# Kernel tuning notes

Measured on AMD Instinct MI355X. Metric: run time of the kernel, lower is better.

The kernel has to match this reference:

```python
import jax, jax.numpy as jnp
import numpy as np

N, E, IN_FT, OUT_FT = 20000, 4096, 128, 128


def setup_inputs() -> dict:
    key = jax.random.key(0)
    kx, kh, kw = jax.random.split(key, 3)
    X = jax.random.normal(kx, (N, IN_FT), dtype=jnp.float32)
    H = jax.random.randint(kh, (N, E), 0, 2, dtype=jnp.int32)
    weight = jax.random.normal(kw, (IN_FT, OUT_FT), dtype=jnp.float32) * (1.0 / np.sqrt(IN_FT))
    bias = jnp.zeros((OUT_FT,), dtype=jnp.float32)
    return {"X": X, "H": H, "weight": weight, "bias": bias}


def reference(X, H, weight, bias):
    # Dv^{-1/2} H De^{-1} H^T Dv^{-1/2} X W + b, with diag matrices fused as
    # row/column scalings (same math as the torch.diag @ chain, no NxN temporaries).
    Hf = H.astype(jnp.float32)
    v_deg = jnp.sum(Hf, axis=1)            # [N]
    e_deg = jnp.sum(Hf, axis=0)            # [E]
    v_deg = jnp.where(v_deg > 0, v_deg, 1.0)
    e_deg = jnp.where(e_deg > 0, e_deg, 1.0)
    dv_inv_sqrt = 1.0 / jnp.sqrt(v_deg)    # diag(Dv^-1/2)
    de_inv = 1.0 / e_deg                   # diag(De^-1)
    Y = dv_inv_sqrt[:, None] * X
    T = Hf.T @ Y                           # H^T (...)        [E, in]
    T = de_inv[:, None] * T                # De^-1 (...)
    Z = Hf @ T                             # H (...)          [N, in]
    Z = dv_inv_sqrt[:, None] * Z           # Dv^-1/2 (...)
    out = Z @ weight + bias                # [N, out]
    return out
```

## Files before the change

kernel.cpp:

```cpp
#include <hip/hip_runtime.h>

#define NV 20000
#define NE 4096
#define FT 128
#define NW_E 128
#define NW_V 625
#define PT_STRIDE 632
#define NKC 313

typedef __attribute__((ext_vector_type(8))) short short8v;
typedef __attribute__((ext_vector_type(4))) float float4v;

__device__ __forceinline__ unsigned short f2bf(float f) {
    unsigned u = __float_as_uint(f);
    u += 0x7FFFu + ((u >> 16) & 1u);
    return (unsigned short)(u >> 16);
}
__device__ __forceinline__ int lds_off(int r, int chunk) {
    return r * 128 + ((chunk ^ (r & 7)) << 4);
}
__device__ __forceinline__ uint4 lut_entry(int t) {
    uint4 e;
    e.x = ((t & 1) ? 0x3F80u : 0u) | ((t & 2) ? 0x3F800000u : 0u);
    e.y = ((t & 4) ? 0x3F80u : 0u) | ((t & 8) ? 0x3F800000u : 0u);
    e.z = ((t & 16) ? 0x3F80u : 0u) | ((t & 32) ? 0x3F800000u : 0u);
    e.w = ((t & 64) ? 0x3F80u : 0u) | ((t & 128) ? 0x3F800000u : 0u);
    return e;
}

__global__ __launch_bounds__(256) void k_pack(const int* __restrict__ H,
                                              unsigned* __restrict__ packed,
                                              float* __restrict__ dv) {
    __shared__ int cl[4];
    int t = threadIdx.x, wave = t >> 6, lane = t & 63;
    int row = blockIdx.x * 2 + (wave >> 1);
    int half = wave & 1;
    const uint4* base = reinterpret_cast<const uint4*>(H) + (size_t)row * 1024 + half * 512 + lane * 8;
    unsigned m = 0;
#pragma unroll
    for (int i = 0; i < 8; ++i) {
        uint4 v = base[i];
        m |= (v.x ? 1u : 0u) << (i * 4 + 0);
        m |= (v.y ? 1u : 0u) << (i * 4 + 1);
        m |= (v.z ? 1u : 0u) << (i * 4 + 2);
        m |= (v.w ? 1u : 0u) << (i * 4 + 3);
    }
    packed[(size_t)row * NW_E + half * 64 + lane] = m;
    int c = __popc(m);
    for (int o = 32; o > 0; o >>= 1) c += __shfl_down(c, o, 64);
    if (lane == 0) cl[wave] = c;
    __syncthreads();
    if (t < 2) {
        int d = cl[t * 2] + cl[t * 2 + 1];
        dv[blockIdx.x * 2 + t] = d > 0 ? 1.0f / sqrtf((float)d) : 1.0f;
    }
}

__global__ __launch_bounds__(256) void k_btrans(const unsigned* __restrict__ packed,
                                                unsigned* __restrict__ packedT) {
    int lane = threadIdx.x & 63;
    int w = threadIdx.x >> 6;
    int ew = blockIdx.y * 4 + w;
    int n = blockIdx.x * 64 + lane;
    unsigned wv = (n < NV) ? packed[(size_t)n * NW_E + ew] : 0u;
    unsigned my = 0;
#pragma unroll
    for (int j = 0; j < 32; ++j) {
        unsigned long long m = __ballot(((wv >> j) & 1u) != 0);
        unsigned part = (lane < 32) ? (unsigned)m : (unsigned)(m >> 32);
        if ((lane & 31) == j) my = part;
    }
    int nw = blockIdx.x * 2 + (lane >> 5);
    int e = ew * 32 + (lane & 31);
    if (nw <= 625) packedT[(size_t)e * PT_STRIDE + nw] = my;
}

__global__ __launch_bounds__(256) void k_mid(const unsigned* __restrict__ packedT,
                                             const float* __restrict__ X,
                                             const float* __restrict__ dv,
                                             float* __restrict__ de,
                                             unsigned short* __restrict__ At) {
    int b = blockIdx.x, t = threadIdx.x;
    int wave = t >> 6, lane = t & 63;
    if (b < 1024) {
        int e = b * 4 + wave;
        const unsigned* row = packedT + (size_t)e * PT_STRIDE;
        int c = 0;
        for (int i = lane; i < NW_V; i += 64) c += __popc(row[i]);
        for (int o = 32; o > 0; o >>= 1) c += __shfl_down(c, o, 64);
        if (lane == 0) de[e] = c > 0 ? 1.0f / (float)c : 1.0f;
    } else if (b < 2274) {
        int b2 = b - 1024;
        int f = t & 127;
        int nb = (b2 * 2 + (t >> 7)) * 8;
        unsigned short h[8];
#pragma unroll
        for (int i = 0; i < 8; ++i) {
            int n = nb + i;
            h[i] = f2bf(X[(size_t)n * FT + f] * dv[n]);
        }
        uint4 u;
        u.x = (unsigned)h[0] | ((unsigned)h[1] << 16);
        u.y = (unsigned)h[2] | ((unsigned)h[3] << 16);
        u.z = (unsigned)h[4] | ((unsigned)h[5] << 16);
        u.w = (unsigned)h[6] | ((unsigned)h[7] << 16);
        int kc = nb >> 6;
        *reinterpret_cast<uint4*>(At + (size_t)kc * 8192 + f * 64 + (nb & 63)) = u;
    } else {
        int f = t & 127;
        uint4 z = {0, 0, 0, 0};
        *reinterpret_cast<uint4*>(At + (size_t)312 * 8192 + f * 64 + 32 + (t >> 7) * 8) = z;
        *reinterpret_cast<uint4*>(At + (size_t)312 * 8192 + f * 64 + 48 + (t >> 7) * 8) = z;
    }
}

__global__ __launch_bounds__(256, 2) void k_mm1(const unsigned short* __restrict__ At,
                                                const unsigned* __restrict__ packedT,
                                                float* __restrict__ P, int chunkK) {
    __shared__ __align__(16) unsigned char sA[16384];
    __shared__ __align__(16) unsigned char sB[16384];
    __shared__ __align__(16) uint4 slut[256];
    int t = threadIdx.x;
    slut[t] = lut_entry(t);

    int et = blockIdx.x & 31, kp = blockIdx.x >> 5;
    int e0 = et * 128;
    int kbeg = kp * chunkK;
    int kend = kbeg + chunkK; if (kend > NKC * 64) kend = NKC * 64;
    int iters = (kend - kbeg) >> 6; if (iters < 0) iters = 0;

    float4v acc[4][4];
#pragma unroll
    for (int i = 0; i < 4; ++i)
#pragma unroll
        for (int j = 0; j < 4; ++j)
#pragma unroll
            for (int r = 0; r < 4; ++r) acc[i][j][r] = 0.0f;

    int wave = t >> 6, lane = t & 63;
    int wm0 = (wave & 1) * 64, wc0 = (wave >> 1) * 64;
    int r0 = lane & 15, q = lane >> 4;

    const unsigned* brow = packedT + (size_t)(e0 + (t & 127)) * PT_STRIDE + (kbeg >> 5);
    uint4 bw, bw2;
    if (t < 128) bw = *reinterpret_cast<const uint4*>(brow);
    __syncthreads();

    for (int it = 0; it < iters; ++it) {
        int kc = (kbeg >> 6) + it;
        const uint4* slab = reinterpret_cast<const uint4*>(At + (size_t)kc * 8192);
#pragma unroll
        for (int c = 0; c < 4; ++c) {
            int idx = c * 256 + t;
            uint4 v = slab[idx];
            *reinterpret_cast<uint4*>(sA + lds_off(idx >> 3, idx & 7)) = v;
        }
        if (t < 128) {
            unsigned w0, w1;
            if (!(it & 1)) {
                bw2 = *reinterpret_cast<const uint4*>(brow + 2 * it + 4);
                w0 = bw.x; w1 = bw.y;
            } else {
                w0 = bw.z; w1 = bw.w;
            }
            int rB = t;
#pragma unroll
            for (int c = 0; c < 4; ++c)
                *reinterpret_cast<uint4*>(sB + lds_off(rB, c)) = slut[(w0 >> (c * 8)) & 0xFF];
#pragma unroll
            for (int c = 0; c < 4; ++c)
                *reinterpret_cast<uint4*>(sB + lds_off(rB, 4 + c)) = slut[(w1 >> (c * 8)) & 0xFF];
            if (it & 1) bw = bw2;
        }
        __syncthreads();
#pragma unroll
        for (int ks = 0; ks < 2; ++ks) {
            short8v a[4], bb[4];
#pragma unroll
            for (int mi = 0; mi < 4; ++mi)
                a[mi] = *reinterpret_cast<const short8v*>(sA + lds_off(wm0 + mi * 16 + r0, ks * 4 + q));
#pragma unroll
            for (int ci = 0; ci < 4; ++ci)
                bb[ci] = *reinterpret_cast<const short8v*>(sB + lds_off(wc0 + ci * 16 + r0, ks * 4 + q));
#pragma unroll
            for (int mi = 0; mi < 4; ++mi)
#pragma unroll
                for (int ci = 0; ci < 4; ++ci)
                    acc[mi][ci] = __builtin_amdgcn_mfma_f32_16x16x32_bf16(a[mi], bb[ci], acc[mi][ci], 0, 0, 0);
        }
        __syncthreads();
    }
    float* Pp = P + (size_t)kp * (128 * 4096);
#pragma unroll
    for (int mi = 0; mi < 4; ++mi)
#pragma unroll
        for (int ci = 0; ci < 4; ++ci) {
            int f = wm0 + mi * 16 + q * 4;
            int e = e0 + wc0 + ci * 16 + r0;
#pragma unroll
            for (int r = 0; r < 4; ++r)
                Pp[(size_t)(f + r) * 4096 + e] = acc[mi][ci][r];
        }
}

__global__ __launch_bounds__(256) void k_reduce(const float4v* __restrict__ P,
                                                float4v* __restrict__ Tt, int S) {
    int i = blockIdx.x * 256 + threadIdx.x;
    float4v a = P[i];
    for (int p = 1; p < S; ++p) a += P[(size_t)p * 131072 + i];
    Tt[i] = a;
}

__global__ __launch_bounds__(256) void k_ut(const float* __restrict__ Tt,
                                            const float* __restrict__ W,
                                            const float* __restrict__ de,
                                            unsigned short* __restrict__ Ut) {
    int t = threadIdx.x;
    int bx = blockIdx.x;
    int e = bx * 64 + (t & 63);
    int g0 = blockIdx.y * 16 + (t >> 6) * 4;
    float a0 = 0, a1 = 0, a2 = 0, a3 = 0;
    for (int f = 0; f < 128; ++f) {
        float tv = Tt[(size_t)f * 4096 + e];
        float4 wv = *reinterpret_cast<const float4*>(W + f * 128 + g0);
        a0 += tv * wv.x; a1 += tv * wv.y; a2 += tv * wv.z; a3 += tv * wv.w;
    }
    float d = de[e];
    int j = t & 63;
    Ut[(size_t)bx * 8192 + (g0 + 0) * 64 + j] = f2bf(a0 * d);
    Ut[(size_t)bx * 8192 + (g0 + 1) * 64 + j] = f2bf(a1 * d);
    Ut[(size_t)bx * 8192 + (g0 + 2) * 64 + j] = f2bf(a2 * d);
    Ut[(size_t)bx * 8192 + (g0 + 3) * 64 + j] = f2bf(a3 * d);
}

__global__ __launch_bounds__(256, 4) void k_mm2(const unsigned* __restrict__ packed,
                                                const unsigned short* __restrict__ Ut,
                                                const float* __restrict__ dv,
                                                const float* __restrict__ bias,
                                                float* __restrict__ out) {
    __shared__ __align__(16) unsigned char sA[16384];
    __shared__ __align__(16) unsigned char sB[4096];
    __shared__ __align__(16) uint4 slut[256];
    int t = threadIdx.x;
    slut[t] = lut_entry(t);

    int mt = blockIdx.x >> 2, qg = blockIdx.x & 3;
    int n0 = mt * 128, g0 = qg * 32;

    float4v acc[4];
#pragma unroll
    for (int i = 0; i < 4; ++i)
#pragma unroll
        for (int r = 0; r < 4; ++r) acc[i][r] = 0.0f;

    int wave = t >> 6, lane = t & 63;
    int wm0 = (wave & 1) * 64, wc0 = (wave >> 1) * 16;
    int r0 = lane & 15, q = lane >> 4;

    const unsigned* arow = packed + (size_t)(n0 + (t & 127)) * NW_E;
    const unsigned short* bbase = Ut + (size_t)qg * 2048;
    int t2 = t - 128;
    uint4 aw, aw2;
    if (t < 128) aw = *reinterpret_cast<const uint4*>(arow);
    __syncthreads();

    for (int it = 0; it < 64; ++it) {
        if (t < 128) {
            unsigned w0, w1;
            if (!(it & 1)) {
                aw2 = *reinterpret_cast<const uint4*>(arow + 2 * it + 4);
                w0 = aw.x; w1 = aw.y;
            } else {
                w0 = aw.z; w1 = aw.w;
            }
            int rA = t;
#pragma unroll
            for (int c = 0; c < 4; ++c)
                *reinterpret_cast<uint4*>(sA + lds_off(rA, c)) = slut[(w0 >> (c * 8)) & 0xFF];
#pragma unroll
            for (int c = 0; c < 4; ++c)
                *reinterpret_cast<uint4*>(sA + lds_off(rA, 4 + c)) = slut[(w1 >> (c * 8)) & 0xFF];
            if (it & 1) aw = aw2;
        } else {
            const uint4* src = reinterpret_cast<const uint4*>(bbase + (size_t)it * 8192);
#pragma unroll
            for (int c = 0; c < 2; ++c) {
                int idx = t2 * 2 + c;
                uint4 v = src[idx];
                *reinterpret_cast<uint4*>(sB + lds_off(idx >> 3, idx & 7)) = v;
            }
        }
        __syncthreads();
#pragma unroll
        for (int ks = 0; ks < 2; ++ks) {
            short8v a[4], bb;
#pragma unroll
            for (int mi = 0; mi < 4; ++mi)
                a[mi] = *reinterpret_cast<const short8v*>(sA + lds_off(wm0 + mi * 16 + r0, ks * 4 + q));
            bb = *reinterpret_cast<const short8v*>(sB + lds_off(wc0 + r0, ks * 4 + q));
#pragma unroll
            for (int mi = 0; mi < 4; ++mi)
                acc[mi] = __builtin_amdgcn_mfma_f32_16x16x32_bf16(a[mi], bb, acc[mi], 0, 0, 0);
        }
        __syncthreads();
    }
    {
        int g = g0 + wc0 + r0;
        float bg = bias[g];
#pragma unroll
        for (int mi = 0; mi < 4; ++mi) {
#pragma unroll
            for (int r = 0; r < 4; ++r) {
                int n = n0 + wm0 + mi * 16 + q * 4 + r;
                if (n < NV) out[(size_t)n * 128 + g] = dv[n] * acc[mi][r] + bg;
            }
        }
    }
}

extern "C" void kernel_launch(void* const* d_in, const int* in_sizes, int n_in,
                              void* d_out, int out_size, void* d_ws, size_t ws_size,
                              hipStream_t stream) {
    const float* X    = (const float*)d_in[0];
    const int*   H    = (const int*)d_in[1];
    const float* W    = (const float*)d_in[2];
    const float* bias = (const float*)d_in[3];
    float* out = (float*)d_out;

    char* ws = (char*)d_ws;
    size_t off = 0;
    auto alloc = [&](size_t sz) { char* p = ws + off; off += (sz + 255) & ~(size_t)255; return p; };
    unsigned*       packed  = (unsigned*)alloc((size_t)NV * NW_E * 4);
    unsigned*       packedT = (unsigned*)alloc((size_t)NE * PT_STRIDE * 4);
    unsigned short* At      = (unsigned short*)alloc((size_t)NKC * 8192 * 2);
    float*          Tt      = (float*)alloc((size_t)FT * NE * 4);
    unsigned short* Ut      = (unsigned short*)alloc((size_t)FT * NE * 2);
    float*          dv      = (float*)alloc((size_t)NV * 4);
    float*          de      = (float*)alloc((size_t)NE * 4);
    size_t fixed = off;

    long long avail = (long long)ws_size - (long long)fixed;
    int S = (int)(avail / (128LL * 4096 * 4));
    if (S > 16) S = 16;
    if (S < 1) S = 1;
    float* P1 = (float*)(ws + fixed);
    int chunkK = ((NKC * 64 + S * 64 - 1) / (S * 64)) * 64;

    k_pack  <<<NV / 2, 256, 0, stream>>>(H, packed, dv);
    k_btrans<<<dim3(313, 32), 256, 0, stream>>>(packed, packedT);
    k_mid   <<<2275, 256, 0, stream>>>(packedT, X, dv, de, At);
    k_mm1   <<<32 * S, 256, 0, stream>>>(At, packedT, P1, chunkK);
    k_reduce<<<512, 256, 0, stream>>>((const float4v*)P1, (float4v*)Tt, S);
    k_ut    <<<dim3(64, 8), 256, 0, stream>>>(Tt, W, de, Ut);
    k_mm2   <<<628, 256, 0, stream>>>(packed, Ut, dv, bias, out);
}
```

Baseline: 590.7 us.

## Use direct global-to-LDS loads for dense operands and fold edge degrees into transpose

```diff
diff --git a/kernel.cpp b/kernel.cpp
--- a/kernel.cpp
+++ b/kernel.cpp
@@ -26,6 +26,11 @@
     e.z = ((t & 16) ? 0x3F80u : 0u) | ((t & 32) ? 0x3F800000u : 0u);
     e.w = ((t & 64) ? 0x3F80u : 0u) | ((t & 128) ? 0x3F800000u : 0u);
     return e;
+}
+__device__ __forceinline__ void dma16(const void* g, void* l) {
+    __builtin_amdgcn_global_load_lds(
+        (const __attribute__((address_space(1))) unsigned*)g,
+        (__attribute__((address_space(3))) unsigned*)l, 16, 0, 0);
 }
 
 __global__ __launch_bounds__(256) void k_pack(const int* __restrict__ H,
@@ -57,7 +62,8 @@
 }
 
 __global__ __launch_bounds__(256) void k_btrans(const unsigned* __restrict__ packed,
-                                                unsigned* __restrict__ packedT) {
+                                                unsigned* __restrict__ packedT,
+                                                int* __restrict__ edeg) {
     int lane = threadIdx.x & 63;
     int w = threadIdx.x >> 6;
     int ew = blockIdx.y * 4 + w;
@@ -72,27 +78,19 @@
     }
     int nw = blockIdx.x * 2 + (lane >> 5);
     int e = ew * 32 + (lane & 31);
-    if (nw <= 625) packedT[(size_t)e * PT_STRIDE + nw] = my;
-}
-
-__global__ __launch_bounds__(256) void k_mid(const unsigned* __restrict__ packedT,
-                                             const float* __restrict__ X,
+    if (nw <= 625) {
+        packedT[(size_t)e * PT_STRIDE + nw] = my;
+        if (my) atomicAdd(&edeg[e], __popc(my));
+    }
+}
+
+__global__ __launch_bounds__(256) void k_mid(const float* __restrict__ X,
                                              const float* __restrict__ dv,
-                                             float* __restrict__ de,
                                              unsigned short* __restrict__ At) {
     int b = blockIdx.x, t = threadIdx.x;
-    int wave = t >> 6, lane = t & 63;
-    if (b < 1024) {
-        int e = b * 4 + wave;
-        const unsigned* row = packedT + (size_t)e * PT_STRIDE;
-        int c = 0;
-        for (int i = lane; i < NW_V; i += 64) c += __popc(row[i]);
-        for (int o = 32; o > 0; o >>= 1) c += __shfl_down(c, o, 64);
-        if (lane == 0) de[e] = c > 0 ? 1.0f / (float)c : 1.0f;
-    } else if (b < 2274) {
-        int b2 = b - 1024;
+    if (b < 1250) {
         int f = t & 127;
-        int nb = (b2 * 2 + (t >> 7)) * 8;
+        int nb = (b * 2 + (t >> 7)) * 8;
         unsigned short h[8];
 #pragma unroll
         for (int i = 0; i < 8; ++i) {
@@ -104,13 +102,16 @@
         u.y = (unsigned)h[2] | ((unsigned)h[3] << 16);
         u.z = (unsigned)h[4] | ((unsigned)h[5] << 16);
         u.w = (unsigned)h[6] | ((unsigned)h[7] << 16);
-        int kc = nb >> 6;
-        *reinterpret_cast<uint4*>(At + (size_t)kc * 8192 + f * 64 + (nb & 63)) = u;
+        int kc = nb >> 6, ch = (nb & 63) >> 3;
+        *reinterpret_cast<uint4*>((char*)At + (size_t)kc * 16384 + ch * 2048 + f * 16) = u;
     } else {
-        int f = t & 127;
         uint4 z = {0, 0, 0, 0};
-        *reinterpret_cast<uint4*>(At + (size_t)312 * 8192 + f * 64 + 32 + (t >> 7) * 8) = z;
-        *reinterpret_cast<uint4*>(At + (size_t)312 * 8192 + f * 64 + 48 + (t >> 7) * 8) = z;
+#pragma unroll
+        for (int c = 0; c < 2; ++c) {
+            int idx = t * 2 + c;
+            int ch = 4 + (idx >> 7), f = idx & 127;
+            *reinterpret_cast<uint4*>((char*)At + (size_t)312 * 16384 + ch * 2048 + f * 16) = z;
+        }
     }
 }
 
@@ -148,12 +149,12 @@
 
     for (int it = 0; it < iters; ++it) {
         int kc = (kbeg >> 6) + it;
-        const uint4* slab = reinterpret_cast<const uint4*>(At + (size_t)kc * 8192);
-#pragma unroll
-        for (int c = 0; c < 4; ++c) {
-            int idx = c * 256 + t;
-            uint4 v = slab[idx];
-            *reinterpret_cast<uint4*>(sA + lds_off(idx >> 3, idx & 7)) = v;
+        if (wave >= 2) {
+            const char* slabg = (const char*)At + (size_t)kc * 16384 + (wave - 2) * 8192;
+            char* slabl = (char*)sA + (wave - 2) * 8192;
+#pragma unroll
+            for (int i = 0; i < 8; ++i)
+                dma16(slabg + i * 1024 + lane * 16, slabl + i * 1024);
         }
         if (t < 128) {
             unsigned w0, w1;
@@ -178,7 +179,7 @@
             short8v a[4], bb[4];
 #pragma unroll
             for (int mi = 0; mi < 4; ++mi)
-                a[mi] = *reinterpret_cast<const short8v*>(sA + lds_off(wm0 + mi * 16 + r0, ks * 4 + q));
+                a[mi] = *reinterpret_cast<const short8v*>(sA + (ks * 4 + q) * 2048 + (wm0 + mi * 16 + r0) * 16);
 #pragma unroll
             for (int ci = 0; ci < 4; ++ci)
                 bb[ci] = *reinterpret_cast<const short8v*>(sB + lds_off(wc0 + ci * 16 + r0, ks * 4 + q));
@@ -213,11 +214,10 @@
 
 __global__ __launch_bounds__(256) void k_ut(const float* __restrict__ Tt,
                                             const float* __restrict__ W,
-                                            const float* __restrict__ de,
+                                            const int* __restrict__ edeg,
                                             unsigned short* __restrict__ Ut) {
     int t = threadIdx.x;
-    int bx = blockIdx.x;
-    int e = bx * 64 + (t & 63);
+    int e = blockIdx.x * 64 + (t & 63);
     int g0 = blockIdx.y * 16 + (t >> 6) * 4;
     float a0 = 0, a1 = 0, a2 = 0, a3 = 0;
     for (int f = 0; f < 128; ++f) {
@@ -225,12 +225,15 @@
         float4 wv = *reinterpret_cast<const float4*>(W + f * 128 + g0);
         a0 += tv * wv.x; a1 += tv * wv.y; a2 += tv * wv.z; a3 += tv * wv.w;
     }
-    float d = de[e];
-    int j = t & 63;
-    Ut[(size_t)bx * 8192 + (g0 + 0) * 64 + j] = f2bf(a0 * d);
-    Ut[(size_t)bx * 8192 + (g0 + 1) * 64 + j] = f2bf(a1 * d);
-    Ut[(size_t)bx * 8192 + (g0 + 2) * 64 + j] = f2bf(a2 * d);
-    Ut[(size_t)bx * 8192 + (g0 + 3) * 64 + j] = f2bf(a3 * d);
+    int dgi = edeg[e];
+    float d = dgi > 0 ? 1.0f / (float)dgi : 1.0f;
+    int ec = e >> 6, ch = (e & 63) >> 3, e7 = e & 7;
+    int qg = g0 >> 5, gg0 = g0 & 31;
+    size_t base = (size_t)ec * 8192 + qg * 2048 + ch * 256 + e7;
+    Ut[base + (gg0 + 0) * 8] = f2bf(a0 * d);
+    Ut[base + (gg0 + 1) * 8] = f2bf(a1 * d);
+    Ut[base + (gg0 + 2) * 8] = f2bf(a2 * d);
+    Ut[base + (gg0 + 3) * 8] = f2bf(a3 * d);
 }
 
 __global__ __launch_bounds__(256, 4) void k_mm2(const unsigned* __restrict__ packed,
@@ -258,14 +261,14 @@
     int r0 = lane & 15, q = lane >> 4;
 
     const unsigned* arow = packed + (size_t)(n0 + (t & 127)) * NW_E;
-    const unsigned short* bbase = Ut + (size_t)qg * 2048;
-    int t2 = t - 128;
+    const char* bbase = (const char*)Ut + (size_t)qg * 4096 + wave * 1024;
     uint4 aw, aw2;
-    if (t < 128) aw = *reinterpret_cast<const uint4*>(arow);
+    if (t >= 128) aw = *reinterpret_cast<const uint4*>(arow);
     __syncthreads();
 
     for (int it = 0; it < 64; ++it) {
-        if (t < 128) {
+        dma16(bbase + (size_t)it * 16384 + lane * 16, (char*)sB + wave * 1024);
+        if (t >= 128) {
             unsigned w0, w1;
             if (!(it & 1)) {
                 aw2 = *reinterpret_cast<const uint4*>(arow + 2 * it + 4);
@@ -273,7 +276,7 @@
             } else {
                 w0 = aw.z; w1 = aw.w;
             }
-            int rA = t;
+            int rA = t & 127;
 #pragma unroll
             for (int c = 0; c < 4; ++c)
                 *reinterpret_cast<uint4*>(sA + lds_off(rA, c)) = slut[(w0 >> (c * 8)) & 0xFF];
@@ -281,14 +284,6 @@
             for (int c = 0; c < 4; ++c)
                 *reinterpret_cast<uint4*>(sA + lds_off(rA, 4 + c)) = slut[(w1 >> (c * 8)) & 0xFF];
             if (it & 1) aw = aw2;
-        } else {
-            const uint4* src = reinterpret_cast<const uint4*>(bbase + (size_t)it * 8192);
-#pragma unroll
-            for (int c = 0; c < 2; ++c) {
-                int idx = t2 * 2 + c;
-                uint4 v = src[idx];
-                *reinterpret_cast<uint4*>(sB + lds_off(idx >> 3, idx & 7)) = v;
-            }
         }
         __syncthreads();
 #pragma unroll
@@ -297,7 +292,7 @@
 #pragma unroll
             for (int mi = 0; mi < 4; ++mi)
                 a[mi] = *reinterpret_cast<const short8v*>(sA + lds_off(wm0 + mi * 16 + r0, ks * 4 + q));
-            bb = *reinterpret_cast<const short8v*>(sB + lds_off(wc0 + r0, ks * 4 + q));
+            bb = *reinterpret_cast<const short8v*>(sB + (ks * 4 + q) * 512 + (wc0 + r0) * 16);
 #pragma unroll
             for (int mi = 0; mi < 4; ++mi)
                 acc[mi] = __builtin_amdgcn_mfma_f32_16x16x32_bf16(a[mi], bb, acc[mi], 0, 0, 0);
@@ -336,7 +331,7 @@
     float*          Tt      = (float*)alloc((size_t)FT * NE * 4);
     unsigned short* Ut      = (unsigned short*)alloc((size_t)FT * NE * 2);
     float*          dv      = (float*)alloc((size_t)NV * 4);
-    float*          de      = (float*)alloc((size_t)NE * 4);
+    int*            edeg    = (int*)alloc((size_t)NE * 4);
     size_t fixed = off;
 
     long long avail = (long long)ws_size - (long long)fixed;
@@ -346,11 +341,12 @@
     float* P1 = (float*)(ws + fixed);
     int chunkK = ((NKC * 64 + S * 64 - 1) / (S * 64)) * 64;
 
+    hipMemsetAsync(edeg, 0, (size_t)NE * 4, stream);
     k_pack  <<<NV / 2, 256, 0, stream>>>(H, packed, dv);
-    k_btrans<<<dim3(313, 32), 256, 0, stream>>>(packed, packedT);
-    k_mid   <<<2275, 256, 0, stream>>>(packedT, X, dv, de, At);
+    k_btrans<<<dim3(313, 32), 256, 0, stream>>>(packed, packedT, edeg);
+    k_mid   <<<1251, 256, 0, stream>>>(X, dv, At);
     k_mm1   <<<32 * S, 256, 0, stream>>>(At, packedT, P1, chunkK);
     k_reduce<<<512, 256, 0, stream>>>((const float4v*)P1, (float4v*)Tt, S);
-    k_ut    <<<dim3(64, 8), 256, 0, stream>>>(Tt, W, de, Ut);
+    k_ut    <<<dim3(64, 8), 256, 0, stream>>>(Tt, W, edeg, Ut);
     k_mm2   <<<628, 256, 0, stream>>>(packed, Ut, dv, bias, out);
 }
```

New measurement: 654.6 us. +10.8%, slower.

## Expand bit-packed incidence to bf16 in registers and fuse edge-degree count

Applied to the files above, without the earlier changes.

```diff
diff --git a/kernel.cpp b/kernel.cpp
--- a/kernel.cpp
+++ b/kernel.cpp
@@ -19,13 +19,16 @@
 __device__ __forceinline__ int lds_off(int r, int chunk) {
     return r * 128 + ((chunk ^ (r & 7)) << 4);
 }
-__device__ __forceinline__ uint4 lut_entry(int t) {
-    uint4 e;
-    e.x = ((t & 1) ? 0x3F80u : 0u) | ((t & 2) ? 0x3F800000u : 0u);
-    e.y = ((t & 4) ? 0x3F80u : 0u) | ((t & 8) ? 0x3F800000u : 0u);
-    e.z = ((t & 16) ? 0x3F80u : 0u) | ((t & 32) ? 0x3F800000u : 0u);
-    e.w = ((t & 64) ? 0x3F80u : 0u) | ((t & 128) ? 0x3F800000u : 0u);
-    return e;
+__device__ __forceinline__ short8v expand8(unsigned b) {
+    union { unsigned u[4]; short8v s; } r;
+#pragma unroll
+    for (int j = 0; j < 4; ++j) {
+        unsigned lo = 0u - (b & 1u);
+        unsigned hi = 0u - (b & 2u);
+        r.u[j] = (lo & 0x3F80u) | (hi & 0x3F800000u);
+        b >>= 2;
+    }
+    return r.s;
 }
 
 __global__ __launch_bounds__(256) void k_pack(const int* __restrict__ H,
@@ -57,7 +60,8 @@
 }
 
 __global__ __launch_bounds__(256) void k_btrans(const unsigned* __restrict__ packed,
-                                                unsigned* __restrict__ packedT) {
+                                                unsigned* __restrict__ packedT,
+                                                int* __restrict__ edeg) {
     int lane = threadIdx.x & 63;
     int w = threadIdx.x >> 6;
     int ew = blockIdx.y * 4 + w;
@@ -72,27 +76,19 @@
     }
     int nw = blockIdx.x * 2 + (lane >> 5);
     int e = ew * 32 + (lane & 31);
-    if (nw <= 625) packedT[(size_t)e * PT_STRIDE + nw] = my;
-}
-
-__global__ __launch_bounds__(256) void k_mid(const unsigned* __restrict__ packedT,
-                                             const float* __restrict__ X,
+    if (nw <= 625) {
+        packedT[(size_t)e * PT_STRIDE + nw] = my;
+        if (my) atomicAdd(&edeg[e], __popc(my));
+    }
+}
+
+__global__ __launch_bounds__(256) void k_mid(const float* __restrict__ X,
                                              const float* __restrict__ dv,
-                                             float* __restrict__ de,
                                              unsigned short* __restrict__ At) {
     int b = blockIdx.x, t = threadIdx.x;
-    int wave = t >> 6, lane = t & 63;
-    if (b < 1024) {
-        int e = b * 4 + wave;
-        const unsigned* row = packedT + (size_t)e * PT_STRIDE;
-        int c = 0;
-        for (int i = lane; i < NW_V; i += 64) c += __popc(row[i]);
-        for (int o = 32; o > 0; o >>= 1) c += __shfl_down(c, o, 64);
-        if (lane == 0) de[e] = c > 0 ? 1.0f / (float)c : 1.0f;
-    } else if (b < 2274) {
-        int b2 = b - 1024;
+    if (b < 1250) {
         int f = t & 127;
-        int nb = (b2 * 2 + (t >> 7)) * 8;
+        int nb = (b * 2 + (t >> 7)) * 8;
         unsigned short h[8];
 #pragma unroll
         for (int i = 0; i < 8; ++i) {
@@ -118,10 +114,8 @@
                                                 const unsigned* __restrict__ packedT,
                                                 float* __restrict__ P, int chunkK) {
     __shared__ __align__(16) unsigned char sA[16384];
-    __shared__ __align__(16) unsigned char sB[16384];
-    __shared__ __align__(16) uint4 slut[256];
+    __shared__ __align__(8) unsigned char sBbits[1024];
     int t = threadIdx.x;
-    slut[t] = lut_entry(t);
 
     int et = blockIdx.x & 31, kp = blockIdx.x >> 5;
     int e0 = et * 128;
@@ -139,12 +133,11 @@
 
     int wave = t >> 6, lane = t & 63;
     int wm0 = (wave & 1) * 64, wc0 = (wave >> 1) * 64;
-    int r0 = lane & 15, q = lane >> 4;
+    int r0 = lane & 15, q = lane >> 4, qs = q * 8;
 
     const unsigned* brow = packedT + (size_t)(e0 + (t & 127)) * PT_STRIDE + (kbeg >> 5);
     uint4 bw, bw2;
     if (t < 128) bw = *reinterpret_cast<const uint4*>(brow);
-    __syncthreads();
 
     for (int it = 0; it < iters; ++it) {
         int kc = (kbeg >> 6) + it;
@@ -156,37 +149,35 @@
             *reinterpret_cast<uint4*>(sA + lds_off(idx >> 3, idx & 7)) = v;
         }
         if (t < 128) {
-            unsigned w0, w1;
+            uint2 wpair;
             if (!(it & 1)) {
                 bw2 = *reinterpret_cast<const uint4*>(brow + 2 * it + 4);
-                w0 = bw.x; w1 = bw.y;
+                wpair.x = bw.x; wpair.y = bw.y;
             } else {
-                w0 = bw.z; w1 = bw.w;
-            }
-            int rB = t;
-#pragma unroll
-            for (int c = 0; c < 4; ++c)
-                *reinterpret_cast<uint4*>(sB + lds_off(rB, c)) = slut[(w0 >> (c * 8)) & 0xFF];
-#pragma unroll
-            for (int c = 0; c < 4; ++c)
-                *reinterpret_cast<uint4*>(sB + lds_off(rB, 4 + c)) = slut[(w1 >> (c * 8)) & 0xFF];
-            if (it & 1) bw = bw2;
+                wpair.x = bw.z; wpair.y = bw.w;
+                bw = bw2;
+            }
+            *reinterpret_cast<uint2*>(sBbits + t * 8) = wpair;
         }
         __syncthreads();
+        uint2 bv[4];
+#pragma unroll
+        for (int ci = 0; ci < 4; ++ci)
+            bv[ci] = *reinterpret_cast<const uint2*>(sBbits + (wc0 + ci * 16 + r0) * 8);
 #pragma unroll
         for (int ks = 0; ks < 2; ++ks) {
-            short8v a[4], bb[4];
+            short8v a[4];
 #pragma unroll
             for (int mi = 0; mi < 4; ++mi)
                 a[mi] = *reinterpret_cast<const short8v*>(sA + lds_off(wm0 + mi * 16 + r0, ks * 4 + q));
 #pragma unroll
-            for (int ci = 0; ci < 4; ++ci)
-                bb[ci] = *reinterpret_cast<const short8v*>(sB + lds_off(wc0 + ci * 16 + r0, ks * 4 + q));
-#pragma unroll
-            for (int mi = 0; mi < 4; ++mi)
-#pragma unroll
-                for (int ci = 0; ci < 4; ++ci)
-                    acc[mi][ci] = __builtin_amdgcn_mfma_f32_16x16x32_bf16(a[mi], bb[ci], acc[mi][ci], 0, 0, 0);
+            for (int ci = 0; ci < 4; ++ci) {
+                unsigned byte = ((ks ? bv[ci].y : bv[ci].x) >> qs) & 0xFFu;
+                short8v bb = expand8(byte);
+#pragma unroll
+                for (int mi = 0; mi < 4; ++mi)
+                    acc[mi][ci] = __builtin_amdgcn_mfma_f32_16x16x32_bf16(a[mi], bb, acc[mi][ci], 0, 0, 0);
+            }
         }
         __syncthreads();
     }
@@ -213,7 +204,7 @@
 
 __global__ __launch_bounds__(256) void k_ut(const float* __restrict__ Tt,
                                             const float* __restrict__ W,
-                                            const float* __restrict__ de,
+                                            const int* __restrict__ edeg,
                                             unsigned short* __restrict__ Ut) {
     int t = threadIdx.x;
     int bx = blockIdx.x;
@@ -225,7 +216,8 @@
         float4 wv = *reinterpret_cast<const float4*>(W + f * 128 + g0);
         a0 += tv * wv.x; a1 += tv * wv.y; a2 += tv * wv.z; a3 += tv * wv.w;
     }
-    float d = de[e];
+    int dgi = edeg[e];
+    float d = dgi > 0 ? 1.0f / (float)dgi : 1.0f;
     int j = t & 63;
     Ut[(size_t)bx * 8192 + (g0 + 0) * 64 + j] = f2bf(a0 * d);
     Ut[(size_t)bx * 8192 + (g0 + 1) * 64 + j] = f2bf(a1 * d);
@@ -238,11 +230,9 @@
                                                 const float* __restrict__ dv,
                                                 const float* __restrict__ bias,
                                                 float* __restrict__ out) {
-    __shared__ __align__(16) unsigned char sA[16384];
+    __shared__ __align__(8) unsigned char sAbits[1024];
     __shared__ __align__(16) unsigned char sB[4096];
-    __shared__ __align__(16) uint4 slut[256];
     int t = threadIdx.x;
-    slut[t] = lut_entry(t);
 
     int mt = blockIdx.x >> 2, qg = blockIdx.x & 3;
     int n0 = mt * 128, g0 = qg * 32;
@@ -255,32 +245,25 @@
 
     int wave = t >> 6, lane = t & 63;
     int wm0 = (wave & 1) * 64, wc0 = (wave >> 1) * 16;
-    int r0 = lane & 15, q = lane >> 4;
+    int r0 = lane & 15, q = lane >> 4, qs = q * 8;
 
     const unsigned* arow = packed + (size_t)(n0 + (t & 127)) * NW_E;
     const unsigned short* bbase = Ut + (size_t)qg * 2048;
     int t2 = t - 128;
     uint4 aw, aw2;
     if (t < 128) aw = *reinterpret_cast<const uint4*>(arow);
-    __syncthreads();
 
     for (int it = 0; it < 64; ++it) {
         if (t < 128) {
-            unsigned w0, w1;
+            uint2 wpair;
             if (!(it & 1)) {
                 aw2 = *reinterpret_cast<const uint4*>(arow + 2 * it + 4);
-                w0 = aw.x; w1 = aw.y;
+                wpair.x = aw.x; wpair.y = aw.y;
             } else {
-                w0 = aw.z; w1 = aw.w;
-            }
-            int rA = t;
-#pragma unroll
-            for (int c = 0; c < 4; ++c)
-                *reinterpret_cast<uint4*>(sA + lds_off(rA, c)) = slut[(w0 >> (c * 8)) & 0xFF];
-#pragma unroll
-            for (int c = 0; c < 4; ++c)
-                *reinterpret_cast<uint4*>(sA + lds_off(rA, 4 + c)) = slut[(w1 >> (c * 8)) & 0xFF];
-            if (it & 1) aw = aw2;
+                wpair.x = aw.z; wpair.y = aw.w;
+                aw = aw2;
+            }
+            *reinterpret_cast<uint2*>(sAbits + t * 8) = wpair;
         } else {
             const uint4* src = reinterpret_cast<const uint4*>(bbase + (size_t)it * 8192);
 #pragma unroll
@@ -291,16 +274,19 @@
             }
         }
         __syncthreads();
+        uint2 av[4];
+#pragma unroll
+        for (int mi = 0; mi < 4; ++mi)
+            av[mi] = *reinterpret_cast<const uint2*>(sAbits + (wm0 + mi * 16 + r0) * 8);
 #pragma unroll
         for (int ks = 0; ks < 2; ++ks) {
-            short8v a[4], bb;
-#pragma unroll
-            for (int mi = 0; mi < 4; ++mi)
-                a[mi] = *reinterpret_cast<const short8v*>(sA + lds_off(wm0 + mi * 16 + r0, ks * 4 + q));
-            bb = *reinterpret_cast<const short8v*>(sB + lds_off(wc0 + r0, ks * 4 + q));
-#pragma unroll
-            for (int mi = 0; mi < 4; ++mi)
-                acc[mi] = __builtin_amdgcn_mfma_f32_16x16x32_bf16(a[mi], bb, acc[mi], 0, 0, 0);
+            short8v bb = *reinterpret_cast<const short8v*>(sB + lds_off(wc0 + r0, ks * 4 + q));
+#pragma unroll
+            for (int mi = 0; mi < 4; ++mi) {
+                unsigned byte = ((ks ? av[mi].y : av[mi].x) >> qs) & 0xFFu;
+                short8v a = expand8(byte);
+                acc[mi] = __builtin_amdgcn_mfma_f32_16x16x32_bf16(a, bb, acc[mi], 0, 0, 0);
+            }
         }
         __syncthreads();
     }
@@ -336,7 +322,7 @@
     float*          Tt      = (float*)alloc((size_t)FT * NE * 4);
     unsigned short* Ut      = (unsigned short*)alloc((size_t)FT * NE * 2);
     float*          dv      = (float*)alloc((size_t)NV * 4);
-    float*          de      = (float*)alloc((size_t)NE * 4);
+    int*            edeg    = (int*)alloc((size_t)NE * 4);
     size_t fixed = off;
 
     long long avail = (long long)ws_size - (long long)fixed;
@@ -346,11 +332,12 @@
     float* P1 = (float*)(ws + fixed);
     int chunkK = ((NKC * 64 + S * 64 - 1) / (S * 64)) * 64;
 
+    hipMemsetAsync(edeg, 0, (size_t)NE * 4, stream);
     k_pack  <<<NV / 2, 256, 0, stream>>>(H, packed, dv);
-    k_btrans<<<dim3(313, 32), 256, 0, stream>>>(packed, packedT);
-    k_mid   <<<2275, 256, 0, stream>>>(packedT, X, dv, de, At);
+    k_btrans<<<dim3(313, 32), 256, 0, stream>>>(packed, packedT, edeg);
+    k_mid   <<<1251, 256, 0, stream>>>(X, dv, At);
     k_mm1   <<<32 * S, 256, 0, stream>>>(At, packedT, P1, chunkK);
     k_reduce<<<512, 256, 0, stream>>>((const float4v*)P1, (float4v*)Tt, S);
-    k_ut    <<<dim3(64, 8), 256, 0, stream>>>(Tt, W, de, Ut);
+    k_ut    <<<dim3(64, 8), 256, 0, stream>>>(Tt, W, edeg, Ut);
     k_mm2   <<<628, 256, 0, stream>>>(packed, Ut, dv, bias, out);
 }
```

Result: slower. 693.7 us (+17.4%).

## Fuse transpose with edge-degree atomics and fold split-K reduce into Ut kernel

Applied to the files above, without the earlier changes.

```diff
diff --git a/kernel.cpp b/kernel.cpp
--- a/kernel.cpp
+++ b/kernel.cpp
@@ -56,61 +56,57 @@
     }
 }
 
-__global__ __launch_bounds__(256) void k_btrans(const unsigned* __restrict__ packed,
-                                                unsigned* __restrict__ packedT) {
-    int lane = threadIdx.x & 63;
-    int w = threadIdx.x >> 6;
-    int ew = blockIdx.y * 4 + w;
-    int n = blockIdx.x * 64 + lane;
-    unsigned wv = (n < NV) ? packed[(size_t)n * NW_E + ew] : 0u;
-    unsigned my = 0;
-#pragma unroll
-    for (int j = 0; j < 32; ++j) {
-        unsigned long long m = __ballot(((wv >> j) & 1u) != 0);
-        unsigned part = (lane < 32) ? (unsigned)m : (unsigned)(m >> 32);
-        if ((lane & 31) == j) my = part;
-    }
-    int nw = blockIdx.x * 2 + (lane >> 5);
-    int e = ew * 32 + (lane & 31);
-    if (nw <= 625) packedT[(size_t)e * PT_STRIDE + nw] = my;
-}
-
-__global__ __launch_bounds__(256) void k_mid(const unsigned* __restrict__ packedT,
-                                             const float* __restrict__ X,
-                                             const float* __restrict__ dv,
-                                             float* __restrict__ de,
-                                             unsigned short* __restrict__ At) {
-    int b = blockIdx.x, t = threadIdx.x;
-    int wave = t >> 6, lane = t & 63;
-    if (b < 1024) {
-        int e = b * 4 + wave;
-        const unsigned* row = packedT + (size_t)e * PT_STRIDE;
-        int c = 0;
-        for (int i = lane; i < NW_V; i += 64) c += __popc(row[i]);
-        for (int o = 32; o > 0; o >>= 1) c += __shfl_down(c, o, 64);
-        if (lane == 0) de[e] = c > 0 ? 1.0f / (float)c : 1.0f;
-    } else if (b < 2274) {
-        int b2 = b - 1024;
-        int f = t & 127;
-        int nb = (b2 * 2 + (t >> 7)) * 8;
-        unsigned short h[8];
-#pragma unroll
-        for (int i = 0; i < 8; ++i) {
-            int n = nb + i;
-            h[i] = f2bf(X[(size_t)n * FT + f] * dv[n]);
-        }
-        uint4 u;
-        u.x = (unsigned)h[0] | ((unsigned)h[1] << 16);
-        u.y = (unsigned)h[2] | ((unsigned)h[3] << 16);
-        u.z = (unsigned)h[4] | ((unsigned)h[5] << 16);
-        u.w = (unsigned)h[6] | ((unsigned)h[7] << 16);
-        int kc = nb >> 6;
-        *reinterpret_cast<uint4*>(At + (size_t)kc * 8192 + f * 64 + (nb & 63)) = u;
+__global__ __launch_bounds__(256) void k_prep(const unsigned* __restrict__ packed,
+                                              const float* __restrict__ X,
+                                              const float* __restrict__ dv,
+                                              unsigned* __restrict__ packedT,
+                                              int* __restrict__ edeg,
+                                              unsigned short* __restrict__ At) {
+    int v = blockIdx.x, t = threadIdx.x;
+    if (v < 10016) {
+        int bx = v % 313, by = v / 313;
+        int lane = t & 63;
+        int w = t >> 6;
+        int ew = by * 4 + w;
+        int n = bx * 64 + lane;
+        unsigned wv = (n < NV) ? packed[(size_t)n * NW_E + ew] : 0u;
+        unsigned my = 0;
+#pragma unroll
+        for (int j = 0; j < 32; ++j) {
+            unsigned long long m = __ballot(((wv >> j) & 1u) != 0);
+            unsigned part = (lane < 32) ? (unsigned)m : (unsigned)(m >> 32);
+            if ((lane & 31) == j) my = part;
+        }
+        int nw = bx * 2 + (lane >> 5);
+        int e = ew * 32 + (lane & 31);
+        if (nw <= 625) {
+            packedT[(size_t)e * PT_STRIDE + nw] = my;
+            if (my) atomicAdd(&edeg[e], __popc(my));
+        }
     } else {
-        int f = t & 127;
-        uint4 z = {0, 0, 0, 0};
-        *reinterpret_cast<uint4*>(At + (size_t)312 * 8192 + f * 64 + 32 + (t >> 7) * 8) = z;
-        *reinterpret_cast<uint4*>(At + (size_t)312 * 8192 + f * 64 + 48 + (t >> 7) * 8) = z;
+        int b = v - 10016;
+        if (b < 1250) {
+            int f = t & 127;
+            int nb = (b * 2 + (t >> 7)) * 8;
+            unsigned short h[8];
+#pragma unroll
+            for (int i = 0; i < 8; ++i) {
+                int n = nb + i;
+                h[i] = f2bf(X[(size_t)n * FT + f] * dv[n]);
+            }
+            uint4 u;
+            u.x = (unsigned)h[0] | ((unsigned)h[1] << 16);
+            u.y = (unsigned)h[2] | ((unsigned)h[3] << 16);
+            u.z = (unsigned)h[4] | ((unsigned)h[5] << 16);
+            u.w = (unsigned)h[6] | ((unsigned)h[7] << 16);
+            int kc = nb >> 6;
+            *reinterpret_cast<uint4*>(At + (size_t)kc * 8192 + f * 64 + (nb & 63)) = u;
+        } else {
+            int f = t & 127;
+            uint4 z = {0, 0, 0, 0};
+            *reinterpret_cast<uint4*>(At + (size_t)312 * 8192 + f * 64 + 32 + (t >> 7) * 8) = z;
+            *reinterpret_cast<uint4*>(At + (size_t)312 * 8192 + f * 64 + 48 + (t >> 7) * 8) = z;
+        }
     }
 }
 
@@ -203,34 +199,49 @@
         }
 }
 
-__global__ __launch_bounds__(256) void k_reduce(const float4v* __restrict__ P,
-                                                float4v* __restrict__ Tt, int S) {
-    int i = blockIdx.x * 256 + threadIdx.x;
-    float4v a = P[i];
-    for (int p = 1; p < S; ++p) a += P[(size_t)p * 131072 + i];
-    Tt[i] = a;
-}
-
-__global__ __launch_bounds__(256) void k_ut(const float* __restrict__ Tt,
-                                            const float* __restrict__ W,
-                                            const float* __restrict__ de,
-                                            unsigned short* __restrict__ Ut) {
+__global__ __launch_bounds__(256) void k_ut2(const float* __restrict__ P,
+                                             const float* __restrict__ W,
+                                             const int* __restrict__ edeg,
+                                             unsigned short* __restrict__ Ut, int S) {
+    __shared__ float sT[128][32];
     int t = threadIdx.x;
-    int bx = blockIdx.x;
-    int e = bx * 64 + (t & 63);
-    int g0 = blockIdx.y * 16 + (t >> 6) * 4;
-    float a0 = 0, a1 = 0, a2 = 0, a3 = 0;
+    int e0 = blockIdx.x * 32;
+    int el = t & 31;
+    int fb = t >> 5;
+    float a[16];
+#pragma unroll
+    for (int i = 0; i < 16; ++i) a[i] = 0.0f;
+    for (int p = 0; p < S; ++p) {
+        const float* Pp = P + (size_t)p * 524288 + e0 + el;
+#pragma unroll
+        for (int i = 0; i < 16; ++i)
+            a[i] += Pp[(size_t)(fb + i * 8) * 4096];
+    }
+#pragma unroll
+    for (int i = 0; i < 16; ++i) sT[fb + i * 8][el] = a[i];
+    __syncthreads();
+    int g0 = (t >> 5) * 16;
+    float acc[16];
+#pragma unroll
+    for (int j = 0; j < 16; ++j) acc[j] = 0.0f;
     for (int f = 0; f < 128; ++f) {
-        float tv = Tt[(size_t)f * 4096 + e];
-        float4 wv = *reinterpret_cast<const float4*>(W + f * 128 + g0);
-        a0 += tv * wv.x; a1 += tv * wv.y; a2 += tv * wv.z; a3 += tv * wv.w;
-    }
-    float d = de[e];
-    int j = t & 63;
-    Ut[(size_t)bx * 8192 + (g0 + 0) * 64 + j] = f2bf(a0 * d);
-    Ut[(size_t)bx * 8192 + (g0 + 1) * 64 + j] = f2bf(a1 * d);
-    Ut[(size_t)bx * 8192 + (g0 + 2) * 64 + j] = f2bf(a2 * d);
-    Ut[(size_t)bx * 8192 + (g0 + 3) * 64 + j] = f2bf(a3 * d);
+        float tv = sT[f][el];
+#pragma unroll
+        for (int j = 0; j < 4; ++j) {
+            float4 wv = *reinterpret_cast<const float4*>(W + f * 128 + g0 + j * 4);
+            acc[j * 4 + 0] += tv * wv.x;
+            acc[j * 4 + 1] += tv * wv.y;
+            acc[j * 4 + 2] += tv * wv.z;
+            acc[j * 4 + 3] += tv * wv.w;
+        }
+    }
+    int e = e0 + el;
+    int dgi = edeg[e];
+    float d = dgi > 0 ? 1.0f / (float)dgi : 1.0f;
+    size_t base = (size_t)(e >> 6) * 8192 + (e & 63);
+#pragma unroll
+    for (int j = 0; j < 16; ++j)
+        Ut[base + (size_t)(g0 + j) * 64] = f2bf(acc[j] * d);
 }
 
 __global__ __launch_bounds__(256, 4) void k_mm2(const unsigned* __restrict__ packed,
@@ -333,10 +344,9 @@
     unsigned*       packed  = (unsigned*)alloc((size_t)NV * NW_E * 4);
     unsigned*       packedT = (unsigned*)alloc((size_t)NE * PT_STRIDE * 4);
     unsigned short* At      = (unsigned short*)alloc((size_t)NKC * 8192 * 2);
-    float*          Tt      = (float*)alloc((size_t)FT * NE * 4);
     unsigned short* Ut      = (unsigned short*)alloc((size_t)FT * NE * 2);
     float*          dv      = (float*)alloc((size_t)NV * 4);
-    float*          de      = (float*)alloc((size_t)NE * 4);
+    int*            edeg    = (int*)alloc((size_t)NE * 4);
     size_t fixed = off;
 
     long long avail = (long long)ws_size - (long long)fixed;
@@ -346,11 +356,10 @@
     float* P1 = (float*)(ws + fixed);
     int chunkK = ((NKC * 64 + S * 64 - 1) / (S * 64)) * 64;
 
-    k_pack  <<<NV / 2, 256, 0, stream>>>(H, packed, dv);
-    k_btrans<<<dim3(313, 32), 256, 0, stream>>>(packed, packedT);
-    k_mid   <<<2275, 256, 0, stream>>>(packedT, X, dv, de, At);
-    k_mm1   <<<32 * S, 256, 0, stream>>>(At, packedT, P1, chunkK);
-    k_reduce<<<512, 256, 0, stream>>>((const float4v*)P1, (float4v*)Tt, S);
-    k_ut    <<<dim3(64, 8), 256, 0, stream>>>(Tt, W, de, Ut);
-    k_mm2   <<<628, 256, 0, stream>>>(packed, Ut, dv, bias, out);
-}
+    hipMemsetAsync(edeg, 0, (size_t)NE * 4, stream);
+    k_pack <<<NV / 2, 256, 0, stream>>>(H, packed, dv);
+    k_prep <<<11267, 256, 0, stream>>>(packed, X, dv, packedT, edeg, At);
+    k_mm1  <<<32 * S, 256, 0, stream>>>(At, packedT, P1, chunkK);
+    k_ut2  <<<128, 256, 0, stream>>>(P1, W, edeg, Ut, S);
+    k_mm2  <<<628, 256, 0, stream>>>(packed, Ut, dv, bias, out);
+}
```

Measured after the change: 666.2 us. +12.8%, slower.
